# Kernel optimization log

Measured on AMD Instinct MI355X. Metric: run time of the kernel, lower is better.

The kernel has to match this reference:

```python
import jax, jax.numpy as jnp
import numpy as np

DEPTH, DIM, DH, QH, KH = 8, 512, 64, 16, 8
B, T, S = 2, 16, 257
NUM_SPECIAL, TBE, CLAMP = 1, 4, 50.0
DI = int(DIM * 4 * 2 / 3)  # 1365
EPS = 1.1920929e-07  # torch.finfo(float32).eps used by torch RMSNorm


def _rms(x, w):
    return x * jax.lax.rsqrt(jnp.mean(jnp.square(x), -1, keepdims=True) + EPS) * w


def _l2norm(x):
    return x / jnp.maximum(jnp.linalg.norm(x, axis=-1, keepdims=True), 1e-12)


def _rotary(n):
    inv = 1.0 / (10000.0 ** (jnp.arange(0, DH, 2, dtype=jnp.float32) / DH))
    f = jnp.arange(n, dtype=jnp.float32)[:, None] * inv[None, :]
    return jnp.concatenate([f, f], -1)  # [n, DH]


def _apply_rot(rot, x):
    x1, x2 = jnp.split(x, 2, -1)
    half = jnp.concatenate([-x2, x1], -1)
    return x * jnp.cos(rot) + half * jnp.sin(rot)


def _attend(q, k, v, mask=None, causal=False):
    # q: [b, QH, n, d]; k, v: [b, KH, n, d]; GQA with groups = QH//KH
    b, hq, n, d = q.shape
    h = k.shape[1]
    g = hq // h
    qg = q.reshape(b, h, g, n, d)
    sim = jnp.einsum('bhgid,bhjd->bhgij', qg, k) * (d ** -0.5)
    sim = jnp.tanh(sim / CLAMP) * CLAMP  # softclamp
    neg = -jnp.finfo(sim.dtype).max
    if mask is not None:
        sim = jnp.where(mask, sim, neg)
    if causal:
        j = sim.shape[-1]
        cm = jnp.triu(jnp.ones((n, j), bool), j - n + 1)
        sim = jnp.where(cm, neg, sim)
    attn = jax.nn.softmax(sim, axis=-1)
    out = jnp.einsum('bhgij,bhjd->bhgid', attn, v)
    return out.reshape(b, hq, n, d)


def _attn_block(x, nw, wq, wk, wv, qg, kg, wo, rot, mask, causal):
    bn, n, _ = x.shape
    h = _rms(x, nw)
    q = (h @ wq).reshape(bn, n, QH, DH).transpose(0, 2, 1, 3)
    k = (h @ wk).reshape(bn, n, KH, DH).transpose(0, 2, 1, 3)
    v = (h @ wv).reshape(bn, n, KH, DH).transpose(0, 2, 1, 3)
    sc = DH ** 0.5
    q = _l2norm(q) * ((qg + 1.0) * sc)[:, None, :]
    k = _l2norm(k) * ((kg + 1.0) * sc)[:, None, :]
    if rot is not None:
        q = _apply_rot(rot, q)
        k = _apply_rot(rot, k)
    o = _attend(q, k, v, mask=mask, causal=causal)
    o = o.transpose(0, 2, 1, 3).reshape(bn, n, QH * DH)
    return o @ wo


def _ff(x, nw, win, bin_, wout, bout):
    h = _rms(x, nw)
    a, g = jnp.split(h @ win + bin_, 2, -1)
    return (a * jax.nn.gelu(g, approximate=False)) @ wout + bout


def setup_inputs() -> dict:
    key = jax.random.key(0)
    ks = jax.random.split(key, 8)
    s = 0.02
    return {
        'tokens': jax.random.normal(ks[0], (B, T, S, DIM), jnp.float32),
        'attn_norm_w': jnp.ones((DEPTH, DIM), jnp.float32),
        'Wq': jax.random.normal(ks[1], (DEPTH, DIM, QH * DH), jnp.float32) * s,
        'Wk': jax.random.normal(ks[2], (DEPTH, DIM, KH * DH), jnp.float32) * s,
        'Wv': jax.random.normal(ks[3], (DEPTH, DIM, KH * DH), jnp.float32) * s,
        'q_gamma': jnp.zeros((DEPTH, QH, DH), jnp.float32),
        'k_gamma': jnp.zeros((DEPTH, KH, DH), jnp.float32),
        'Wo': jax.random.normal(ks[4], (DEPTH, QH * DH, DIM), jnp.float32) * s,
        'ff_norm_w': jnp.ones((DEPTH, DIM), jnp.float32),
        'W_in': jax.random.normal(ks[5], (DEPTH, DIM, 2 * DI), jnp.float32) * s,
        'b_in': jnp.zeros((DEPTH, 2 * DI), jnp.float32),
        'W_out': jax.random.normal(ks[6], (DEPTH, DI, DIM), jnp.float32) * s,
        'b_out': jnp.zeros((DEPTH, DIM), jnp.float32),
        'final_w': jnp.ones((DIM,), jnp.float32),
    }


def reference(tokens, attn_norm_w, Wq, Wk, Wv, q_gamma, k_gamma, Wo,
              ff_norm_w, W_in, b_in, W_out, b_out, final_w):
    x = tokens  # [B, T, S, D]
    # spatial special-token mask: normal tokens cannot attend to special (rightmost) tokens
    idx = jnp.arange(S)
    is_sp = idx >= (S - NUM_SPECIAL)
    sp_mask = ~((~is_sp[:, None]) & is_sp[None, :])  # [S, S]
    sp_mask = sp_mask[None, None, None]  # broadcast over (b, h, g)
    rot = _rotary(T)
    for l in range(DEPTH):
        is_time = (l + 1) % TBE == 0
        if is_time:
            y = x.transpose(0, 2, 1, 3).reshape(B * S, T, DIM)
            o = _attn_block(y, attn_norm_w[l], Wq[l], Wk[l], Wv[l], q_gamma[l],
                            k_gamma[l], Wo[l], rot=rot, mask=None, causal=True)
            x = x + o.reshape(B, S, T, DIM).transpose(0, 2, 1, 3)
        else:
            y = x.reshape(B * T, S, DIM)
            o = _attn_block(y, attn_norm_w[l], Wq[l], Wk[l], Wv[l], q_gamma[l],
                            k_gamma[l], Wo[l], rot=None, mask=sp_mask, causal=False)
            x = x + o.reshape(B, T, S, DIM)
        x = x + _ff(x, ff_norm_w[l], W_in[l], b_in[l], W_out[l], b_out[l])
    return _rms(x, final_w)
```

## Files before the change

kernel.cpp:

```cpp
#include <hip/hip_runtime.h>
#include <hip/hip_bf16.h>
#include <math.h>

typedef __attribute__((ext_vector_type(8))) short short8;
typedef __attribute__((ext_vector_type(4))) float f32x4;
typedef __hip_bfloat16 bf16;

#define BB 2
#define TT 16
#define SSQ 257
#define DIMD 512
#define NROWS 8224
#define DII 1365
#define DI2 2730
#define FNPAD 2816
#define GLULD 1408
#define SKP 288
#define EPSR 1.1920929e-07f

__device__ __forceinline__ void async16(const void* g, const void* l) {
    __builtin_amdgcn_global_load_lds(
        (const __attribute__((address_space(1))) void*)g,
        (__attribute__((address_space(3))) void*)l, 16, 0, 0);
}

__device__ __forceinline__ short f2bfs(float x) {
    bf16 h = __float2bfloat16(x);
    return *reinterpret_cast<short*>(&h);
}

__device__ __forceinline__ float glu_fast(float a, float g) {
    float x = g * 0.70710678118654752f;
    float ax = fabsf(x);
    float t = __builtin_amdgcn_rcpf(__builtin_fmaf(0.3275911f, ax, 1.f));
    float p = t * (0.254829592f + t * (-0.284496736f + t * (1.421413741f
              + t * (-1.453152027f + t * 1.061405429f))));
    float erfv = 1.f - p * __expf(-ax * ax);
    erfv = (x < 0.f) ? -erfv : erfv;
    return a * 0.5f * g * (1.f + erfv);
}

__global__ void wtrans_layer(const float* __restrict__ wq, const float* __restrict__ wk,
                             const float* __restrict__ wv, const float* __restrict__ wo,
                             const float* __restrict__ win, const float* __restrict__ wout,
                             bf16* __restrict__ dqkv, bf16* __restrict__ dwo,
                             bf16* __restrict__ dwin, bf16* __restrict__ dwout) {
    __shared__ float tile[32][33];
    int bid = blockIdx.x;
    const float* src; bf16* dst; int K, M, Kpad, interleave = 0, local;
    if (bid < 512)       { src = wq;   dst = dqkv;            K = 512;  M = 1024; Kpad = 512;  local = bid; }
    else if (bid < 768)  { src = wk;   dst = dqkv + 1024*512; K = 512;  M = 512;  Kpad = 512;  local = bid - 512; }
    else if (bid < 1024) { src = wv;   dst = dqkv + 1536*512; K = 512;  M = 512;  Kpad = 512;  local = bid - 768; }
    else if (bid < 1536) { src = wo;   dst = dwo;             K = 1024; M = 512;  Kpad = 1024; local = bid - 1024; }
    else if (bid < 2944) { src = win;  dst = dwin;            K = 512;  M = 2730; Kpad = 512;  local = bid - 1536; interleave = 1; }
    else                 { src = wout; dst = dwout;           K = 1365; M = 512;  Kpad = 1408; local = bid - 2944; }
    int tilesx = Kpad >> 5;
    int k0 = (local % tilesx) * 32, m0 = (local / tilesx) * 32;
    int tx = threadIdx.x & 31, ty = threadIdx.x >> 5;
    #pragma unroll
    for (int i = 0; i < 4; ++i) {
        int k = k0 + ty + 8 * i, m = m0 + tx;
        tile[ty + 8 * i][tx] = (k < K && m < M) ? src[(size_t)k * M + m] : 0.f;
    }
    __syncthreads();
    #pragma unroll
    for (int i = 0; i < 4; ++i) {
        int n = m0 + ty + 8 * i, k = k0 + tx;
        int nd = n;
        if (interleave) {
            if (n < DII)        nd = ((n >> 4) << 5) + (n & 15);
            else if (n < DI2) { int m = n - DII; nd = ((m >> 4) << 5) + 16 + (m & 15); }
            else              { int q = n - DI2; int j = DII + (q >> 1);
                                nd = ((j >> 4) << 5) + ((q & 1) << 4) + (j & 15); }
        }
        dst[(size_t)nd * Kpad + k] = __float2bfloat16(tile[tx][ty + 8 * i]);
    }
}

template<int BF16OUT>
__global__ __launch_bounds__(256)
void rms_kernel(const float* __restrict__ x, const float* __restrict__ w,
                void* __restrict__ out, int perm) {
    int wave = threadIdx.x >> 6, lane = threadIdx.x & 63;
    int r = blockIdx.x * 4 + wave;
    int src = r;
    if (perm) {
        int t = r & 15; int rs = r >> 4; int s = rs % SSQ; int b = rs / SSQ;
        src = (b * TT + t) * SSQ + s;
    }
    const float4* xr = (const float4*)(x + (size_t)src * DIMD) + lane * 2;
    float4 a = xr[0], c = xr[1];
    float ss = a.x*a.x + a.y*a.y + a.z*a.z + a.w*a.w
             + c.x*c.x + c.y*c.y + c.z*c.z + c.w*c.w;
    ss += __shfl_xor(ss, 1);  ss += __shfl_xor(ss, 2);  ss += __shfl_xor(ss, 4);
    ss += __shfl_xor(ss, 8);  ss += __shfl_xor(ss, 16); ss += __shfl_xor(ss, 32);
    float sc = rsqrtf(ss * (1.f / DIMD) + EPSR);
    const float4* wr = (const float4*)w + lane * 2;
    float4 wa = wr[0], wb = wr[1];
    if (BF16OUT) {
        short8 v;
        v[0] = f2bfs(a.x * sc * wa.x); v[1] = f2bfs(a.y * sc * wa.y);
        v[2] = f2bfs(a.z * sc * wa.z); v[3] = f2bfs(a.w * sc * wa.w);
        v[4] = f2bfs(c.x * sc * wb.x); v[5] = f2bfs(c.y * sc * wb.y);
        v[6] = f2bfs(c.z * sc * wb.z); v[7] = f2bfs(c.w * sc * wb.w);
        *(short8*)((bf16*)out + (size_t)r * DIMD + lane * 8) = v;
    } else {
        float4* o = (float4*)((float*)out + (size_t)r * DIMD) + lane * 2;
        float4 o0 = {a.x * sc * wa.x, a.y * sc * wa.y, a.z * sc * wa.z, a.w * sc * wa.w};
        float4 o1 = {c.x * sc * wb.x, c.y * sc * wb.y, c.z * sc * wb.z, c.w * sc * wb.w};
        o[0] = o0; o[1] = o1;
    }
}

template<int EPI>
__global__ __launch_bounds__(512, 1)
void mfma_gemm_panel(const bf16* __restrict__ A, int lda,
                     const bf16* __restrict__ Bt, int ldb,
                     const float* __restrict__ bias,
                     void* __restrict__ C, int ldc,
                     int nrow, int mchunk,
                     const float* __restrict__ qg, const float* __restrict__ kg,
                     int rotary) {
    __shared__ __align__(16) short lds_b[128 * 512];
    int gx = gridDim.x;
    int nwg = gx * gridDim.y;
    int lin = blockIdx.y * gx + blockIdx.x;
    int q8 = nwg >> 3, r8 = nwg & 7;
    int xcd = lin & 7, idx = lin >> 3;
    int wsw = (xcd < r8 ? xcd * (q8 + 1) : r8 * (q8 + 1) + (xcd - r8) * q8) + idx;
    int bx = wsw % gx, by = wsw / gx;
    int n0 = bx * 128, m0 = by * mchunk;

    int tid = threadIdx.x;
    int wave = tid >> 6, lane = tid & 63;
    int quad = lane >> 4, l16 = lane & 15;

    const short* Bp = (const short*)Bt;
    #pragma unroll
    for (int j = 0; j < 16; ++j) {
        int gi = tid + 512 * j;
        int n = gi & 127, c = gi >> 7;
        async16(Bp + (size_t)(n0 + n) * ldb + c * 8, &lds_b[gi * 8]);
    }
    const short* Ap = (const short*)A;

    float gl[2][4];
    float c0r[4], s0r[4], c1r[4], s1r[4];
    bool isqk = false;
    float ba[4], bg[4];
    if constexpr (EPI == 1) {
        int headb = n0 >> 6;
        isqk = headb < 24;
        if (isqk) {
            #pragma unroll
            for (int hh = 0; hh < 2; ++hh) {
                int head = headb + hh;
                const float* g = head < 16 ? qg + head * 64 : kg + (head - 16) * 64;
                gl[hh][0] = (g[l16] + 1.f) * 8.f;
                gl[hh][1] = (g[16 + l16] + 1.f) * 8.f;
                gl[hh][2] = (g[32 + l16] + 1.f) * 8.f;
                gl[hh][3] = (g[48 + l16] + 1.f) * 8.f;
            }
        }
        if (rotary) {
            float inv0 = __expf(-(float)l16 * 0.28782313662425572f);
            float inv1 = __expf(-(float)(l16 + 16) * 0.28782313662425572f);
            #pragma unroll
            for (int e = 0; e < 4; ++e) {
                float t = (float)(quad * 4 + e);
                c0r[e] = __cosf(t * inv0); s0r[e] = __sinf(t * inv0);
                c1r[e] = __cosf(t * inv1); s1r[e] = __sinf(t * inv1);
            }
        }
    } else {
        int jb = n0 >> 1;
        #pragma unroll
        for (int t = 0; t < 4; ++t) {
            int j = jb + t * 16 + l16;
            ba[t] = (j < DII) ? bias[j] : 0.f;
            bg[t] = (j < DII) ? bias[DII + j] : 0.f;
        }
    }
    __syncthreads();

    int base_b = (quad * 128 + l16) * 16;
    int nfrag = mchunk >> 4;
    for (int f = wave; f < nfrag; f += 8) {
        int mrow = m0 + f * 16 + l16;
        if (mrow >= nrow) mrow = nrow - 1;
        const short* ap = Ap + (size_t)mrow * lda + quad * 8;
        f32x4 acc[8];
        #pragma unroll
        for (int nj = 0; nj < 8; ++nj) acc[nj] = {0.f, 0.f, 0.f, 0.f};
        short8 a = *(const short8*)ap;
        short8 anext = a;
        #pragma unroll
        for (int kt = 0; kt < 16; ++kt) {
            if (kt < 15) anext = *(const short8*)(ap + (kt + 1) * 32);
            const char* vb = (const char*)lds_b + base_b + kt * 8192;
            __builtin_amdgcn_s_setprio(1);
            #pragma unroll
            for (int nj = 0; nj < 8; ++nj) {
                short8 b = *(const short8*)(vb + nj * 256);
                acc[nj] = __builtin_amdgcn_mfma_f32_16x16x32_bf16(a, b, acc[nj], 0, 0, 0);
            }
            __builtin_amdgcn_s_setprio(0);
            a = anext;
        }
        if constexpr (EPI == 1) {
            #pragma unroll
            for (int hh = 0; hh < 2; ++hh) {
                #pragma unroll
                for (int e = 0; e < 4; ++e) {
                    int row = m0 + f * 16 + quad * 4 + e;
                    float v0 = acc[hh * 4 + 0][e], v1 = acc[hh * 4 + 1][e];
                    float v2 = acc[hh * 4 + 2][e], v3 = acc[hh * 4 + 3][e];
                    if (isqk) {
                        float ss = v0 * v0 + v1 * v1 + v2 * v2 + v3 * v3;
                        ss += __shfl_xor(ss, 1); ss += __shfl_xor(ss, 2);
                        ss += __shfl_xor(ss, 4); ss += __shfl_xor(ss, 8);
                        float invn = 1.f / fmaxf(sqrtf(ss), 1e-12f);
                        v0 *= invn * gl[hh][0]; v1 *= invn * gl[hh][1];
                        v2 *= invn * gl[hh][2]; v3 *= invn * gl[hh][3];
                        if (rotary) {
                            float n0v = v0 * c0r[e] - v2 * s0r[e];
                            float n1v = v1 * c1r[e] - v3 * s1r[e];
                            float n2v = v2 * c0r[e] + v0 * s0r[e];
                            float n3v = v3 * c1r[e] + v1 * s1r[e];
                            v0 = n0v; v1 = n1v; v2 = n2v; v3 = n3v;
                        }
                    }
                    if (row < nrow) {
                        bf16* p = (bf16*)C + (size_t)row * ldc + n0 + hh * 64 + l16;
                        p[0]  = __float2bfloat16(v0);
                        p[16] = __float2bfloat16(v1);
                        p[32] = __float2bfloat16(v2);
                        p[48] = __float2bfloat16(v3);
                    }
                }
            }
        } else {
            int jb = n0 >> 1;
            #pragma unroll
            for (int e = 0; e < 4; ++e) {
                int row = m0 + f * 16 + quad * 4 + e;
                if (row < nrow) {
                    bf16* cr = (bf16*)C + (size_t)row * ldc;
                    #pragma unroll
                    for (int t = 0; t < 4; ++t)
                        cr[jb + t * 16 + l16] = __float2bfloat16(
                            glu_fast(acc[2 * t][e] + ba[t], acc[2 * t + 1][e] + bg[t]));
                }
            }
        }
    }
}

template<int EPI, int PERM, int TM>
__global__ __launch_bounds__(256)
void mfma_gemm(const bf16* __restrict__ A, int lda,
               const bf16* __restrict__ Bt, int ldb,
               const float* __restrict__ bias,
               void* __restrict__ C, int ldc, int Mstore,
               int nrow, int K) {
    constexpr int MI = TM / 32;
    constexpr int ALW = TM / 64;
    __shared__ __align__(16) short lds_a[2][TM * 32];
    __shared__ __align__(16) short lds_b[2][128 * 32];
    int tid = threadIdx.x;
    int wave = tid >> 6, lane = tid & 63;
    int quad = lane >> 4, l16 = lane & 15;
    int m0 = blockIdx.y * TM, n0 = blockIdx.x * 128;
    int wm = (wave & 1) * (TM / 2), wn = (wave >> 1) * 64;
    f32x4 zero4 = {0.f, 0.f, 0.f, 0.f};
    f32x4 acc[MI][4];
    #pragma unroll
    for (int i = 0; i < MI; ++i)
        #pragma unroll
        for (int j = 0; j < 4; ++j) acc[i][j] = zero4;

    const short* Ap = (const short*)A;
    const short* Bp = (const short*)Bt;
    auto aptr = [&](int g) {
        int m = g >> 2, kc = (g & 3) ^ ((g >> 3) & 3);
        int r = m0 + m; if (r >= nrow) r = nrow - 1;
        return Ap + (size_t)r * lda + kc * 8;
    };
    auto bptr = [&](int g) {
        int m = g >> 2, kc = (g & 3) ^ ((g >> 3) & 3);
        return Bp + (size_t)(n0 + m) * ldb + kc * 8;
    };
    const short* gA[ALW]; int aoff[ALW];
    #pragma unroll
    for (int j = 0; j < ALW; ++j) {
        gA[j] = aptr(wave * TM + j * 64 + lane);
        aoff[j] = (wave * TM + j * 64) * 8;
    }
    const short* gB0 = bptr(wave * 128 + lane);
    const short* gB1 = bptr(wave * 128 + 64 + lane);
    int boff0 = (wave * 128) * 8, boff1 = (wave * 128 + 64) * 8;

    auto stage = [&](int buf, int kt) {
        int ko = kt * 32;
        #pragma unroll
        for (int j = 0; j < ALW; ++j)
            async16(gA[j] + ko, &lds_a[buf][aoff[j]]);
        async16(gB0 + ko, &lds_b[buf][boff0]);
        async16(gB1 + ko, &lds_b[buf][boff1]);
    };

    int nk = K >> 5;
    stage(0, 0);
    for (int kt = 0; kt < nk; ++kt) {
        int buf = kt & 1;
        __syncthreads();
        if (kt + 1 < nk) stage(buf ^ 1, kt + 1);
        short8 af[MI], bfr[4];
        #pragma unroll
        for (int mi = 0; mi < MI; ++mi) {
            int m = wm + mi * 16 + l16;
            af[mi] = *(const short8*)&lds_a[buf][(m * 4 + (quad ^ ((m >> 1) & 3))) * 8];
        }
        #pragma unroll
        for (int nj = 0; nj < 4; ++nj) {
            int n = wn + nj * 16 + l16;
            bfr[nj] = *(const short8*)&lds_b[buf][(n * 4 + (quad ^ ((n >> 1) & 3))) * 8];
        }
        #pragma unroll
        for (int mi = 0; mi < MI; ++mi)
            #pragma unroll
            for (int nj = 0; nj < 4; ++nj)
                acc[mi][nj] = __builtin_amdgcn_mfma_f32_16x16x32_bf16(
                    af[mi], bfr[nj], acc[mi][nj], 0, 0, 0);
    }

    #pragma unroll
    for (int mi = 0; mi < MI; ++mi) {
        #pragma unroll
        for (int e = 0; e < 4; ++e) {
            int row = m0 + wm + mi * 16 + quad * 4 + e;
            if (row >= nrow) continue;
            int orow = row;
            if (PERM) {
                int t = row & 15; int rs = row >> 4; int s = rs % SSQ; int b = rs / SSQ;
                orow = (b * TT + t) * SSQ + s;
            }
            #pragma unroll
            for (int nj = 0; nj < 4; ++nj) {
                int col = n0 + wn + nj * 16 + l16;
                if (col >= Mstore) continue;
                float v = acc[mi][nj][e];
                if (bias) v += bias[col];
                ((float*)C)[(size_t)orow * ldc + col] += v;
            }
        }
    }
}

__global__ void vtrans_kernel(const bf16* __restrict__ qkv, bf16* __restrict__ vt) {
    int bkh = blockIdx.x;
    int kc = blockIdx.y;
    int bt = bkh >> 3, kh = bkh & 7;
    int tid = threadIdx.x;
    #pragma unroll
    for (int i = 0; i < 8; ++i) {
        int idx = tid + 256 * i;
        int kl = idx >> 6;
        int d = idx & 63;
        int key = kc * 32 + kl;
        float v = 0.f;
        if (key < SSQ)
            v = __bfloat162float(qkv[((size_t)(bt * SSQ + key)) * 2048 + 1536 + kh * 64 + d]);
        vt[((size_t)bkh * 64 + d) * SKP + key] = __float2bfloat16(v);
    }
}

__global__ __launch_bounds__(256)
void space_attn_kernel(const bf16* __restrict__ qkv, const bf16* __restrict__ vt,
                       bf16* __restrict__ ob) {
    __shared__ __align__(16) short kls[272 * 8 * 8];
    int qt = blockIdx.x, qh = blockIdx.y, bt = blockIdx.z;
    int kh = qh >> 1;
    int tid = threadIdx.x, wave = tid >> 6, lane = tid & 63;
    int quad = lane >> 4, l16 = lane & 15;
    int q0w = qt * 64 + wave * 16;
    int q = q0w + l16;
    int qc = q > 256 ? 256 : q;
    const short* qbase = (const short*)qkv + (size_t)bt * SSQ * 2048;

    const short* kgbase = qbase + 1024 + kh * 64;
    #pragma unroll
    for (int it = 0; it < 9; ++it) {
        int u = it * 4 + wave;
        if (u < 34) {
            int g = u * 64 + lane;
            int key = g >> 3, ch = g & 7;
            int srck = key < SSQ ? key : 256;
            async16(kgbase + (size_t)srck * 2048 + (ch ^ (key & 7)) * 8,
                    &kls[u * 512]);
        }
    }

    const short* qp = qbase + (size_t)qc * 2048 + qh * 64;
    short8 bq0 = *(const short8*)(qp + quad * 8);
    short8 bq1 = *(const short8*)(qp + 32 + quad * 8);
    __syncthreads();

    f32x4 zero4 = {0.f, 0.f, 0.f, 0.f};
    f32x4 sc[18];
    float sum = 0.f;
    int c0 = quad ^ (l16 & 7);
    #pragma unroll
    for (int kt = 0; kt < 17; ++kt) {
        int key = kt * 16 + l16;
        short8 ak0 = *(const short8*)&kls[(key * 8 + c0) * 8];
        short8 ak1 = *(const short8*)&kls[(key * 8 + (c0 ^ 4)) * 8];
        f32x4 cc = zero4;
        cc = __builtin_amdgcn_mfma_f32_16x16x32_bf16(ak0, bq0, cc, 0, 0, 0);
        cc = __builtin_amdgcn_mfma_f32_16x16x32_bf16(ak1, bq1, cc, 0, 0, 0);
        #pragma unroll
        for (int e = 0; e < 4; ++e) {
            float x = cc[e] * 0.0025f;
            float x2 = x * x;
            float v = cc[e] * 0.125f * (1.f + x2 * (-0.3333333333f + x2 * 0.1333333333f));
            float p = __expf(v);
            if (kt == 16) {
                bool valid = (e == 0) && (quad == 0) && (q == 256);
                p = valid ? p : 0.f;
            }
            cc[e] = p;
            sum += p;
        }
        sc[kt] = cc;
    }
    #pragma unroll
    for (int e = 0; e < 4; ++e) sc[17][e] = 0.f;
    sum += __shfl_xor(sum, 16);
    sum += __shfl_xor(sum, 32);
    float inv = __builtin_amdgcn_rcpf(sum);
    f32x4 inv4;
    #pragma unroll
    for (int e = 0; e < 4; ++e) inv4[e] = __shfl(inv, quad * 4 + e);

    f32x4 oacc[4];
    #pragma unroll
    for (int nt = 0; nt < 4; ++nt) oacc[nt] = zero4;
    const short* vbp = (const short*)vt + ((size_t)(bt * 8 + kh) * 64 + l16) * SKP;
    #pragma unroll
    for (int c8 = 0; c8 < 9; ++c8) {
        short8 pb;
        #pragma unroll
        for (int j = 0; j < 8; ++j) {
            int src_lane = ((quad & 1) * 2 + (j >> 2)) * 16 + l16;
            float v0 = __shfl(sc[2 * c8][j & 3], src_lane);
            float v1 = __shfl(sc[2 * c8 + 1][j & 3], src_lane);
            pb[j] = f2bfs(quad < 2 ? v0 : v1);
        }
        #pragma unroll
        for (int nt = 0; nt < 4; ++nt) {
            short8 av = *(const short8*)(vbp + (size_t)(nt * 16) * SKP + c8 * 32 + quad * 8);
            oacc[nt] = __builtin_amdgcn_mfma_f32_16x16x32_bf16(pb, av, oacc[nt], 0, 0, 0);
        }
    }

    #pragma unroll
    for (int e = 0; e < 4; ++e) {
        int qq = q0w + quad * 4 + e;
        if (qq <= 256) {
            bf16* op = ob + ((size_t)(bt * SSQ + qq)) * 1024 + qh * 64 + l16;
            float s = inv4[e];
            op[0]  = __float2bfloat16(oacc[0][e] * s);
            op[16] = __float2bfloat16(oacc[1][e] * s);
            op[32] = __float2bfloat16(oacc[2][e] * s);
            op[48] = __float2bfloat16(oacc[3][e] * s);
        }
    }
}

__global__ void time_attn_kernel(const bf16* __restrict__ qkv, bf16* __restrict__ ob) {
    __shared__ float qs[16][65], ks[16][65], ps[16][17];
    int bs = blockIdx.x, qh = blockIdx.y, kh = qh >> 1;
    int tid = threadIdx.x;
    size_t rowbase = (size_t)bs * 16;
    #pragma unroll
    for (int i = 0; i < 4; ++i) {
        int idx = tid + 256 * i;
        int r = idx >> 6, d = idx & 63;
        qs[r][d] = __bfloat162float(qkv[(rowbase + r) * 2048 + qh * 64 + d]);
        ks[r][d] = __bfloat162float(qkv[(rowbase + r) * 2048 + 1024 + kh * 64 + d]);
    }
    __syncthreads();
    int i = tid >> 4, j = tid & 15;
    float dot = 0.f;
    #pragma unroll 16
    for (int d = 0; d < 64; ++d) dot += qs[i][d] * ks[j][d];
    float s = dot * 0.125f;
    float x = s * 0.02f;
    float x2 = x * x;
    float v = s * (1.f + x2 * (-0.3333333333f + x2 * 0.1333333333f));
    float p = (j > i) ? 0.f : __expf(v);
    float sum = p;
    sum += __shfl_xor(sum, 1);
    sum += __shfl_xor(sum, 2);
    sum += __shfl_xor(sum, 4);
    sum += __shfl_xor(sum, 8);
    ps[i][j] = p * __builtin_amdgcn_rcpf(sum);
    __syncthreads();
    #pragma unroll
    for (int ii = 0; ii < 4; ++ii) {
        int idx = tid + 256 * ii;
        int r = idx >> 6, d = idx & 63;
        float acc = 0.f;
        #pragma unroll
        for (int jj = 0; jj < 16; ++jj)
            acc += ps[r][jj] * __bfloat162float(qkv[(rowbase + jj) * 2048 + 1536 + kh * 64 + d]);
        ob[(rowbase + r) * 1024 + qh * 64 + d] = __float2bfloat16(acc);
    }
}

extern "C" void kernel_launch(void* const* d_in, const int* in_sizes, int n_in,
                              void* d_out, int out_size, void* d_ws, size_t ws_size,
                              hipStream_t stream) {
    const float* tokens      = (const float*)d_in[0];
    const float* attn_norm_w = (const float*)d_in[1];
    const float* Wq          = (const float*)d_in[2];
    const float* Wk          = (const float*)d_in[3];
    const float* Wv          = (const float*)d_in[4];
    const float* q_gamma     = (const float*)d_in[5];
    const float* k_gamma     = (const float*)d_in[6];
    const float* Wo          = (const float*)d_in[7];
    const float* ff_norm_w   = (const float*)d_in[8];
    const float* W_in        = (const float*)d_in[9];
    const float* b_in        = (const float*)d_in[10];
    const float* W_out       = (const float*)d_in[11];
    const float* b_out       = (const float*)d_in[12];
    const float* final_w     = (const float*)d_in[13];

    float* x = (float*)d_out;
    char* ws = (char*)d_ws;

    bf16* wtqkv = (bf16*)ws;
    bf16* wto   = wtqkv + 2048 * 512;
    bf16* wtin  = wto   + 512 * 1024;
    bf16* wtout = wtin  + 2816 * 512;
    size_t off = (size_t)(2048*512 + 512*1024 + 2816*512 + 512*1408) * 2;
    bf16* h = (bf16*)(ws + off);
    off += (size_t)NROWS * 512 * 2;
    char* region = ws + off;
    bf16* qkv = (bf16*)region;
    bf16* glu = (bf16*)region;
    bf16* vt  = (bf16*)(region + (size_t)NROWS * 2048 * 2);
    bf16* ob  = (bf16*)(region + (size_t)NROWS * 2048 * 2 + (size_t)256*64*SKP*2);

    hipMemcpyAsync(x, tokens, (size_t)NROWS * 512 * 4, hipMemcpyDeviceToDevice, stream);

    for (int l = 0; l < 8; ++l) {
        int is_time = ((l + 1) % 4 == 0) ? 1 : 0;
        wtrans_layer<<<3648, 256, 0, stream>>>(
            Wq + (size_t)l * 512 * 1024, Wk + (size_t)l * 512 * 512,
            Wv + (size_t)l * 512 * 512, Wo + (size_t)l * 1024 * 512,
            W_in + (size_t)l * 512 * DI2, W_out + (size_t)l * DII * 512,
            wtqkv, wto, wtin, wtout);

        rms_kernel<1><<<2056, 256, 0, stream>>>(x, attn_norm_w + (size_t)l * 512, h, is_time);
        mfma_gemm_panel<1><<<dim3(16, 16), 512, 0, stream>>>(
            h, 512, wtqkv, 512, nullptr, qkv, 2048, NROWS, 528,
            q_gamma + (size_t)l * 1024, k_gamma + (size_t)l * 512, is_time);
        if (is_time) {
            time_attn_kernel<<<dim3(514, 16), 256, 0, stream>>>(qkv, ob);
            mfma_gemm<3, 1, 64><<<dim3(4, 129), 256, 0, stream>>>(
                ob, 1024, wto, 1024, nullptr, x, 512, 512, NROWS, 1024);
        } else {
            vtrans_kernel<<<dim3(256, 9), 256, 0, stream>>>(qkv, vt);
            space_attn_kernel<<<dim3(5, 16, 32), 256, 0, stream>>>(qkv, vt, ob);
            mfma_gemm<3, 0, 64><<<dim3(4, 129), 256, 0, stream>>>(
                ob, 1024, wto, 1024, nullptr, x, 512, 512, NROWS, 1024);
        }

        rms_kernel<1><<<2056, 256, 0, stream>>>(x, ff_norm_w + (size_t)l * 512, h, 0);
        mfma_gemm_panel<2><<<dim3(22, 11), 512, 0, stream>>>(
            h, 512, wtin, 512, b_in + (size_t)l * DI2, glu, GLULD, NROWS, 768,
            nullptr, nullptr, 0);
        mfma_gemm<3, 0, 64><<<dim3(4, 129), 256, 0, stream>>>(
            glu, GLULD, wtout, GLULD, b_out + (size_t)l * 512, x, 512, 512, NROWS, GLULD);
    }

    rms_kernel<0><<<2056, 256, 0, stream>>>(x, final_w, x, 0);
}
```

Before: 2.057 ms.

## Replace accumulate GEMMs with LDS-resident B panel kernel and MFMA time attention

The output-projection and FF-down GEMMs now use a new kernel that loads a 64-column slice of the transposed weight fully into LDS (up to 128KB). Each wave then streams A rows directly from global memory with register prefetch, and workgroups are swizzled across XCDs. The FF-down GEMM is split into two K-chunk launches (1024 + 384) because of the LDS size limit, and both accumulate into x in fp32. The time attention kernel is rewritten to use MFMA for QK^T and PV, with four heads per block and K/V staged in LDS. This replaces the scalar LDS dot products. The trade-off is single-block occupancy per CU, and the split launches add an extra read-modify-write of x.

```diff
diff --git a/kernel.cpp b/kernel.cpp
--- a/kernel.cpp
+++ b/kernel.cpp
@@ -256,103 +256,76 @@
     }
 }
 
-template<int EPI, int PERM, int TM>
-__global__ __launch_bounds__(256)
-void mfma_gemm(const bf16* __restrict__ A, int lda,
-               const bf16* __restrict__ Bt, int ldb,
-               const float* __restrict__ bias,
-               void* __restrict__ C, int ldc, int Mstore,
-               int nrow, int K) {
-    constexpr int MI = TM / 32;
-    constexpr int ALW = TM / 64;
-    __shared__ __align__(16) short lds_a[2][TM * 32];
-    __shared__ __align__(16) short lds_b[2][128 * 32];
+__global__ __launch_bounds__(512, 1)
+void mfma_panel_acc(const bf16* __restrict__ A, int lda, int koff, int K,
+                    const bf16* __restrict__ Bt, int ldb,
+                    const float* __restrict__ bias,
+                    float* __restrict__ C, int ldc,
+                    int nrow, int mchunk, int perm) {
+    __shared__ __align__(16) short lds_b[64 * 1024];
+    int gx = gridDim.x;
+    int nwg = gx * gridDim.y;
+    int lin = blockIdx.y * gx + blockIdx.x;
+    int q8 = nwg >> 3, r8 = nwg & 7;
+    int xcd = lin & 7, idx = lin >> 3;
+    int wsw = (xcd < r8 ? xcd * (q8 + 1) : r8 * (q8 + 1) + (xcd - r8) * q8) + idx;
+    int bx = wsw % gx, by = wsw / gx;
+    int n0 = bx * 64, m0 = by * mchunk;
+
     int tid = threadIdx.x;
     int wave = tid >> 6, lane = tid & 63;
     int quad = lane >> 4, l16 = lane & 15;
-    int m0 = blockIdx.y * TM, n0 = blockIdx.x * 128;
-    int wm = (wave & 1) * (TM / 2), wn = (wave >> 1) * 64;
-    f32x4 zero4 = {0.f, 0.f, 0.f, 0.f};
-    f32x4 acc[MI][4];
-    #pragma unroll
-    for (int i = 0; i < MI; ++i)
-        #pragma unroll
-        for (int j = 0; j < 4; ++j) acc[i][j] = zero4;
+
+    const short* Bp = (const short*)Bt;
+    int ng = (K >> 3) * 64;
+    for (int gi = tid; gi < ng; gi += 512) {
+        int n = gi & 63, c = gi >> 6;
+        async16(Bp + (size_t)(n0 + n) * ldb + koff + c * 8, &lds_b[gi * 8]);
+    }
+    float bs4[4];
+    #pragma unroll
+    for (int t = 0; t < 4; ++t)
+        bs4[t] = bias ? bias[n0 + t * 16 + l16] : 0.f;
+    __syncthreads();
 
     const short* Ap = (const short*)A;
-    const short* Bp = (const short*)Bt;
-    auto aptr = [&](int g) {
-        int m = g >> 2, kc = (g & 3) ^ ((g >> 3) & 3);
-        int r = m0 + m; if (r >= nrow) r = nrow - 1;
-        return Ap + (size_t)r * lda + kc * 8;
-    };
-    auto bptr = [&](int g) {
-        int m = g >> 2, kc = (g & 3) ^ ((g >> 3) & 3);
-        return Bp + (size_t)(n0 + m) * ldb + kc * 8;
-    };
-    const short* gA[ALW]; int aoff[ALW];
-    #pragma unroll
-    for (int j = 0; j < ALW; ++j) {
-        gA[j] = aptr(wave * TM + j * 64 + lane);
-        aoff[j] = (wave * TM + j * 64) * 8;
-    }
-    const short* gB0 = bptr(wave * 128 + lane);
-    const short* gB1 = bptr(wave * 128 + 64 + lane);
-    int boff0 = (wave * 128) * 8, boff1 = (wave * 128 + 64) * 8;
-
-    auto stage = [&](int buf, int kt) {
-        int ko = kt * 32;
-        #pragma unroll
-        for (int j = 0; j < ALW; ++j)
-            async16(gA[j] + ko, &lds_a[buf][aoff[j]]);
-        async16(gB0 + ko, &lds_b[buf][boff0]);
-        async16(gB1 + ko, &lds_b[buf][boff1]);
-    };
-
     int nk = K >> 5;
-    stage(0, 0);
-    for (int kt = 0; kt < nk; ++kt) {
-        int buf = kt & 1;
-        __syncthreads();
-        if (kt + 1 < nk) stage(buf ^ 1, kt + 1);
-        short8 af[MI], bfr[4];
-        #pragma unroll
-        for (int mi = 0; mi < MI; ++mi) {
-            int m = wm + mi * 16 + l16;
-            af[mi] = *(const short8*)&lds_a[buf][(m * 4 + (quad ^ ((m >> 1) & 3))) * 8];
-        }
-        #pragma unroll
-        for (int nj = 0; nj < 4; ++nj) {
-            int n = wn + nj * 16 + l16;
-            bfr[nj] = *(const short8*)&lds_b[buf][(n * 4 + (quad ^ ((n >> 1) & 3))) * 8];
-        }
-        #pragma unroll
-        for (int mi = 0; mi < MI; ++mi)
+    int nfrag = mchunk >> 4;
+    for (int f = wave; f < nfrag; f += 8) {
+        int mrow = m0 + f * 16 + l16;
+        if (mrow >= nrow) mrow = nrow - 1;
+        const short* ap = Ap + (size_t)mrow * lda + koff + quad * 8;
+        f32x4 acc[4];
+        #pragma unroll
+        for (int nj = 0; nj < 4; ++nj) acc[nj] = {0.f, 0.f, 0.f, 0.f};
+        short8 a = *(const short8*)ap;
+        #pragma unroll 4
+        for (int kt = 0; kt < nk; ++kt) {
+            short8 anext = a;
+            if (kt + 1 < nk) anext = *(const short8*)(ap + (kt + 1) * 32);
+            const char* vb = (const char*)lds_b + ((kt * 4 + quad) * 64 + l16) * 16;
+            __builtin_amdgcn_s_setprio(1);
+            #pragma unroll
+            for (int nj = 0; nj < 4; ++nj) {
+                short8 b = *(const short8*)(vb + nj * 256);
+                acc[nj] = __builtin_amdgcn_mfma_f32_16x16x32_bf16(a, b, acc[nj], 0, 0, 0);
+            }
+            __builtin_amdgcn_s_setprio(0);
+            a = anext;
+        }
+        #pragma unroll
+        for (int e = 0; e < 4; ++e) {
+            int row = m0 + f * 16 + quad * 4 + e;
+            if (row >= nrow) continue;
+            int orow = row;
+            if (perm) {
+                int t = row & 15; int rs = row >> 4; int s = rs % SSQ; int b = rs / SSQ;
+                orow = (b * TT + t) * SSQ + s;
+            }
+            float* cr = C + (size_t)orow * ldc + n0;
             #pragma unroll
             for (int nj = 0; nj < 4; ++nj)
-                acc[mi][nj] = __builtin_amdgcn_mfma_f32_16x16x32_bf16(
-                    af[mi], bfr[nj], acc[mi][nj], 0, 0, 0);
-    }
-
-    #pragma unroll
-    for (int mi = 0; mi < MI; ++mi) {
-        #pragma unroll
-        for (int e = 0; e < 4; ++e) {
-            int row = m0 + wm + mi * 16 + quad * 4 + e;
-            if (row >= nrow) continue;
-            int orow = row;
-            if (PERM) {
-                int t = row & 15; int rs = row >> 4; int s = rs % SSQ; int b = rs / SSQ;
-                orow = (b * TT + t) * SSQ + s;
-            }
-            #pragma unroll
-            for (int nj = 0; nj < 4; ++nj) {
-                int col = n0 + wn + nj * 16 + l16;
-                if (col >= Mstore) continue;
-                float v = acc[mi][nj][e];
-                if (bias) v += bias[col];
-                ((float*)C)[(size_t)orow * ldc + col] += v;
-            }
+                cr[nj * 16 + l16] += acc[nj][e] + bs4[nj];
         }
     }
 }
@@ -477,44 +450,86 @@
     }
 }
 
-__global__ void time_attn_kernel(const bf16* __restrict__ qkv, bf16* __restrict__ ob) {
-    __shared__ float qs[16][65], ks[16][65], ps[16][17];
-    int bs = blockIdx.x, qh = blockIdx.y, kh = qh >> 1;
-    int tid = threadIdx.x;
+__global__ __launch_bounds__(256)
+void time_attn_kernel(const bf16* __restrict__ qkv, bf16* __restrict__ ob) {
+    __shared__ __align__(16) short kls[2 * 16 * 64];
+    __shared__ __align__(16) short vls[2 * 64 * 24];
+    int bs = blockIdx.x, qg = blockIdx.y;
+    int tid = threadIdx.x, wave = tid >> 6, lane = tid & 63;
+    int quad = lane >> 4, l16 = lane & 15;
+    int qh = qg * 4 + wave;
+    int khl_w = wave >> 1;
     size_t rowbase = (size_t)bs * 16;
-    #pragma unroll
-    for (int i = 0; i < 4; ++i) {
-        int idx = tid + 256 * i;
-        int r = idx >> 6, d = idx & 63;
-        qs[r][d] = __bfloat162float(qkv[(rowbase + r) * 2048 + qh * 64 + d]);
-        ks[r][d] = __bfloat162float(qkv[(rowbase + r) * 2048 + 1024 + kh * 64 + d]);
-    }
+    const short* qbase = (const short*)qkv;
+
+    {
+        int c = tid & 7, key = (tid >> 3) & 15, khl = tid >> 7;
+        const short* ksrc = qbase + (rowbase + key) * 2048 + 1024 + (qg * 2 + khl) * 64
+                            + (c ^ (key & 7)) * 8;
+        async16(ksrc, &kls[((khl * 16 + key) * 8 + c) * 8]);
+        short8 vv = *(const short8*)(qbase + (rowbase + key) * 2048 + 1536
+                                     + (qg * 2 + khl) * 64 + c * 8);
+        #pragma unroll
+        for (int dd = 0; dd < 8; ++dd)
+            vls[(khl * 64 + c * 8 + dd) * 24 + key] = vv[dd];
+    }
+    const short* qp = qbase + (rowbase + l16) * 2048 + qh * 64;
+    short8 bq0 = *(const short8*)(qp + quad * 8);
+    short8 bq1 = *(const short8*)(qp + 32 + quad * 8);
     __syncthreads();
-    int i = tid >> 4, j = tid & 15;
-    float dot = 0.f;
-    #pragma unroll 16
-    for (int d = 0; d < 64; ++d) dot += qs[i][d] * ks[j][d];
-    float s = dot * 0.125f;
-    float x = s * 0.02f;
-    float x2 = x * x;
-    float v = s * (1.f + x2 * (-0.3333333333f + x2 * 0.1333333333f));
-    float p = (j > i) ? 0.f : __expf(v);
-    float sum = p;
-    sum += __shfl_xor(sum, 1);
-    sum += __shfl_xor(sum, 2);
-    sum += __shfl_xor(sum, 4);
-    sum += __shfl_xor(sum, 8);
-    ps[i][j] = p * __builtin_amdgcn_rcpf(sum);
-    __syncthreads();
-    #pragma unroll
-    for (int ii = 0; ii < 4; ++ii) {
-        int idx = tid + 256 * ii;
-        int r = idx >> 6, d = idx & 63;
-        float acc = 0.f;
-        #pragma unroll
-        for (int jj = 0; jj < 16; ++jj)
-            acc += ps[r][jj] * __bfloat162float(qkv[(rowbase + jj) * 2048 + 1536 + kh * 64 + d]);
-        ob[(rowbase + r) * 1024 + qh * 64 + d] = __float2bfloat16(acc);
+
+    int c0 = quad ^ (l16 & 7);
+    const short* kw = &kls[(khl_w * 16 + l16) * 64];
+    short8 ak0 = *(const short8*)(kw + c0 * 8);
+    short8 ak1 = *(const short8*)(kw + (c0 ^ 4) * 8);
+    f32x4 cc = {0.f, 0.f, 0.f, 0.f};
+    cc = __builtin_amdgcn_mfma_f32_16x16x32_bf16(ak0, bq0, cc, 0, 0, 0);
+    cc = __builtin_amdgcn_mfma_f32_16x16x32_bf16(ak1, bq1, cc, 0, 0, 0);
+    float sum = 0.f;
+    #pragma unroll
+    for (int e = 0; e < 4; ++e) {
+        float s = cc[e] * 0.125f;
+        float x = s * 0.02f, x2 = x * x;
+        float v = s * (1.f + x2 * (-0.3333333333f + x2 * 0.1333333333f));
+        float p = ((quad * 4 + e) > l16) ? 0.f : __expf(v);
+        cc[e] = p;
+        sum += p;
+    }
+    sum += __shfl_xor(sum, 16);
+    sum += __shfl_xor(sum, 32);
+    float inv = __builtin_amdgcn_rcpf(sum);
+    f32x4 inv4;
+    #pragma unroll
+    for (int e = 0; e < 4; ++e) inv4[e] = __shfl(inv, quad * 4 + e);
+
+    short8 pa;
+    #pragma unroll
+    for (int jj = 0; jj < 8; ++jj) {
+        int key = quad * 8 + jj;
+        int src = ((key >> 2) & 3) * 16 + l16;
+        float v = __shfl(cc[jj & 3], src);
+        pa[jj] = f2bfs(quad < 2 ? v : 0.f);
+    }
+    const short* vw = &vls[khl_w * 64 * 24];
+    short8 zero8 = {0, 0, 0, 0, 0, 0, 0, 0};
+    f32x4 oacc[4];
+    #pragma unroll
+    for (int nt = 0; nt < 4; ++nt) {
+        short8 av = zero8;
+        if (quad < 2)
+            av = *(const short8*)(vw + (nt * 16 + l16) * 24 + quad * 8);
+        f32x4 z = {0.f, 0.f, 0.f, 0.f};
+        oacc[nt] = __builtin_amdgcn_mfma_f32_16x16x32_bf16(pa, av, z, 0, 0, 0);
+    }
+    #pragma unroll
+    for (int e = 0; e < 4; ++e) {
+        int q = quad * 4 + e;
+        bf16* op = ob + (rowbase + q) * 1024 + qh * 64 + l16;
+        float s = inv4[e];
+        op[0]  = __float2bfloat16(oacc[0][e] * s);
+        op[16] = __float2bfloat16(oacc[1][e] * s);
+        op[32] = __float2bfloat16(oacc[2][e] * s);
+        op[48] = __float2bfloat16(oacc[3][e] * s);
     }
 }
 
@@ -567,22 +582,24 @@
             h, 512, wtqkv, 512, nullptr, qkv, 2048, NROWS, 528,
             q_gamma + (size_t)l * 1024, k_gamma + (size_t)l * 512, is_time);
         if (is_time) {
-            time_attn_kernel<<<dim3(514, 16), 256, 0, stream>>>(qkv, ob);
-            mfma_gemm<3, 1, 64><<<dim3(4, 129), 256, 0, stream>>>(
-                ob, 1024, wto, 1024, nullptr, x, 512, 512, NROWS, 1024);
+            time_attn_kernel<<<dim3(514, 4), 256, 0, stream>>>(qkv, ob);
         } else {
             vtrans_kernel<<<dim3(256, 9), 256, 0, stream>>>(qkv, vt);
             space_attn_kernel<<<dim3(5, 16, 32), 256, 0, stream>>>(qkv, vt, ob);
-            mfma_gemm<3, 0, 64><<<dim3(4, 129), 256, 0, stream>>>(
-                ob, 1024, wto, 1024, nullptr, x, 512, 512, NROWS, 1024);
-        }
+        }
+        mfma_panel_acc<<<dim3(8, 31), 512, 0, stream>>>(
+            ob, 1024, 0, 1024, wto, 1024, nullptr, x, 512, NROWS, 272, is_time);
 
         rms_kernel<1><<<2056, 256, 0, stream>>>(x, ff_norm_w + (size_t)l * 512, h, 0);
         mfma_gemm_panel<2><<<dim3(22, 11), 512, 0, stream>>>(
             h, 512, wtin, 512, b_in + (size_t)l * DI2, glu, GLULD, NROWS, 768,
             nullptr, nullptr, 0);
-        mfma_gemm<3, 0, 64><<<dim3(4, 129), 256, 0, stream>>>(
-            glu, GLULD, wtout, GLULD, b_out + (size_t)l * 512, x, 512, 512, NROWS, GLULD);
+        mfma_panel_acc<<<dim3(8, 31), 512, 0, stream>>>(
+            glu, GLULD, 0, 1024, wtout, GLULD, b_out + (size_t)l * 512, x, 512,
+            NROWS, 272, 0);
+        mfma_panel_acc<<<dim3(8, 31), 512, 0, stream>>>(
+            glu, GLULD, 1024, 384, wtout, GLULD, nullptr, x, 512,
+            NROWS, 272, 0);
     }
 
     rms_kernel<0><<<2056, 256, 0, stream>>>(x, final_w, x, 0);
```

Measured after the change: 2.142 ms. 4.1% more time.

## Fuse V transpose into space attention and rewrite time attention with MFMA

Applied to the files above, without the earlier changes.

The space attention kernel now loads K and transposes V into LDS itself, which removes the separate vtrans kernel and its global round trip. Each block covers one (bt, kh) pair and loops over both query heads of the GQA group, so K/V are staged once per group instead of once per query tile and head. The time attention kernel is rewritten to use bf16 MFMA for QK^T and PV, with one block serving four query heads, in place of the scalar fp32 LDS loops. The costs are fewer blocks for the space kernel (256), larger LDS per block, and a scalar scatter when transposing V.

```diff
diff --git a/kernel.cpp b/kernel.cpp
--- a/kernel.cpp
+++ b/kernel.cpp
@@ -16,6 +16,7 @@
 #define FNPAD 2816
 #define GLULD 1408
 #define SKP 288
+#define SKP2 320
 #define EPSR 1.1920929e-07f
 
 __device__ __forceinline__ void async16(const void* g, const void* l) {
@@ -357,84 +358,177 @@
     }
 }
 
-__global__ void vtrans_kernel(const bf16* __restrict__ qkv, bf16* __restrict__ vt) {
-    int bkh = blockIdx.x;
-    int kc = blockIdx.y;
-    int bt = bkh >> 3, kh = bkh & 7;
-    int tid = threadIdx.x;
-    #pragma unroll
-    for (int i = 0; i < 8; ++i) {
-        int idx = tid + 256 * i;
-        int kl = idx >> 6;
-        int d = idx & 63;
-        int key = kc * 32 + kl;
-        float v = 0.f;
-        if (key < SSQ)
-            v = __bfloat162float(qkv[((size_t)(bt * SSQ + key)) * 2048 + 1536 + kh * 64 + d]);
-        vt[((size_t)bkh * 64 + d) * SKP + key] = __float2bfloat16(v);
-    }
-}
-
-__global__ __launch_bounds__(256)
-void space_attn_kernel(const bf16* __restrict__ qkv, const bf16* __restrict__ vt,
-                       bf16* __restrict__ ob) {
+__global__ __launch_bounds__(512)
+void space_attn_kernel(const bf16* __restrict__ qkv, bf16* __restrict__ ob) {
     __shared__ __align__(16) short kls[272 * 8 * 8];
-    int qt = blockIdx.x, qh = blockIdx.y, bt = blockIdx.z;
-    int kh = qh >> 1;
+    __shared__ __align__(16) short vls[64 * SKP2];
+    int bt = blockIdx.x, kh = blockIdx.y;
     int tid = threadIdx.x, wave = tid >> 6, lane = tid & 63;
     int quad = lane >> 4, l16 = lane & 15;
-    int q0w = qt * 64 + wave * 16;
-    int q = q0w + l16;
-    int qc = q > 256 ? 256 : q;
     const short* qbase = (const short*)qkv + (size_t)bt * SSQ * 2048;
-
     const short* kgbase = qbase + 1024 + kh * 64;
-    #pragma unroll
-    for (int it = 0; it < 9; ++it) {
-        int u = it * 4 + wave;
-        if (u < 34) {
-            int g = u * 64 + lane;
+    const short* vgbase = qbase + 1536 + kh * 64;
+
+    #pragma unroll
+    for (int u = 0; u < 5; ++u) {
+        int g = u * 512 + tid;
+        if (g < 2176) {
             int key = g >> 3, ch = g & 7;
             int srck = key < SSQ ? key : 256;
-            async16(kgbase + (size_t)srck * 2048 + (ch ^ (key & 7)) * 8,
-                    &kls[u * 512]);
-        }
-    }
-
-    const short* qp = qbase + (size_t)qc * 2048 + qh * 64;
+            async16(kgbase + (size_t)srck * 2048 + (ch ^ (key & 7)) * 8, &kls[g * 8]);
+        }
+    }
+    #pragma unroll
+    for (int u = 0; u < 5; ++u) {
+        int g = u * 512 + tid;
+        if (g < 2176) {
+            int key = g >> 3, c = g & 7;
+            int srck = key < SSQ ? key : 256;
+            short8 vv = *(const short8*)(vgbase + (size_t)srck * 2048 + c * 8);
+            int kc = key >> 3, kl = key & 7;
+            #pragma unroll
+            for (int dd = 0; dd < 8; ++dd) {
+                int d = c * 8 + dd;
+                vls[(d * 40 + (kc ^ (d & 7))) * 8 + kl] = vv[dd];
+            }
+        }
+    }
+    if (tid < 128) {
+        int d = tid >> 1, kc = 34 + (tid & 1);
+        short8 z8 = {0, 0, 0, 0, 0, 0, 0, 0};
+        *(short8*)&vls[(d * 40 + (kc ^ (d & 7))) * 8] = z8;
+    }
+    __syncthreads();
+
+    f32x4 zero4 = {0.f, 0.f, 0.f, 0.f};
+    int c0 = quad ^ (l16 & 7);
+    int d7 = l16 & 7;
+    for (int f = wave; f < 34; f += 8) {
+        int qh_l = (f >= 17) ? 1 : 0;
+        int qt = f - qh_l * 17;
+        int qh = kh * 2 + qh_l;
+        int q = qt * 16 + l16;
+        int qc = q > 256 ? 256 : q;
+        const short* qp = qbase + (size_t)qc * 2048 + qh * 64;
+        short8 bq0 = *(const short8*)(qp + quad * 8);
+        short8 bq1 = *(const short8*)(qp + 32 + quad * 8);
+
+        f32x4 sc[18];
+        float sum = 0.f;
+        #pragma unroll
+        for (int kt = 0; kt < 17; ++kt) {
+            int key = kt * 16 + l16;
+            short8 ak0 = *(const short8*)&kls[(key * 8 + c0) * 8];
+            short8 ak1 = *(const short8*)&kls[(key * 8 + (c0 ^ 4)) * 8];
+            f32x4 cc = zero4;
+            cc = __builtin_amdgcn_mfma_f32_16x16x32_bf16(ak0, bq0, cc, 0, 0, 0);
+            cc = __builtin_amdgcn_mfma_f32_16x16x32_bf16(ak1, bq1, cc, 0, 0, 0);
+            #pragma unroll
+            for (int e = 0; e < 4; ++e) {
+                float x = cc[e] * 0.0025f;
+                float x2 = x * x;
+                float v = cc[e] * 0.125f * (1.f + x2 * (-0.3333333333f + x2 * 0.1333333333f));
+                float p = __expf(v);
+                if (kt == 16) {
+                    bool valid = (e == 0) && (quad == 0) && (q == 256);
+                    p = valid ? p : 0.f;
+                }
+                cc[e] = p;
+                sum += p;
+            }
+            sc[kt] = cc;
+        }
+        #pragma unroll
+        for (int e = 0; e < 4; ++e) sc[17][e] = 0.f;
+        sum += __shfl_xor(sum, 16);
+        sum += __shfl_xor(sum, 32);
+        float inv = __builtin_amdgcn_rcpf(sum);
+        f32x4 inv4;
+        #pragma unroll
+        for (int e = 0; e < 4; ++e) inv4[e] = __shfl(inv, quad * 4 + e);
+
+        f32x4 oacc[4];
+        #pragma unroll
+        for (int nt = 0; nt < 4; ++nt) oacc[nt] = zero4;
+        #pragma unroll
+        for (int c8 = 0; c8 < 9; ++c8) {
+            short8 pb;
+            #pragma unroll
+            for (int j = 0; j < 8; ++j) {
+                int src_lane = ((quad & 1) * 2 + (j >> 2)) * 16 + l16;
+                float v0 = __shfl(sc[2 * c8][j & 3], src_lane);
+                float v1 = __shfl(sc[2 * c8 + 1][j & 3], src_lane);
+                pb[j] = f2bfs(quad < 2 ? v0 : v1);
+            }
+            #pragma unroll
+            for (int nt = 0; nt < 4; ++nt) {
+                int d = nt * 16 + l16;
+                int kc = (c8 * 4 + quad) ^ d7;
+                short8 av = *(const short8*)&vls[(d * 40 + kc) * 8];
+                oacc[nt] = __builtin_amdgcn_mfma_f32_16x16x32_bf16(pb, av, oacc[nt], 0, 0, 0);
+            }
+        }
+
+        #pragma unroll
+        for (int e = 0; e < 4; ++e) {
+            int qq = qt * 16 + quad * 4 + e;
+            if (qq <= 256) {
+                bf16* op = ob + ((size_t)(bt * SSQ + qq)) * 1024 + qh * 64 + l16;
+                float s = inv4[e];
+                op[0]  = __float2bfloat16(oacc[0][e] * s);
+                op[16] = __float2bfloat16(oacc[1][e] * s);
+                op[32] = __float2bfloat16(oacc[2][e] * s);
+                op[48] = __float2bfloat16(oacc[3][e] * s);
+            }
+        }
+    }
+}
+
+__global__ __launch_bounds__(256)
+void time_attn_kernel(const bf16* __restrict__ qkv, bf16* __restrict__ ob) {
+    __shared__ __align__(16) short kls[2 * 16 * 64];
+    __shared__ __align__(16) short vls[2 * 64 * 24];
+    int bs = blockIdx.x, qg = blockIdx.y;
+    int tid = threadIdx.x, wave = tid >> 6, lane = tid & 63;
+    int quad = lane >> 4, l16 = lane & 15;
+    int qh = qg * 4 + wave;
+    int khl_w = wave >> 1;
+    size_t rowbase = (size_t)bs * 16;
+    const short* qbase = (const short*)qkv;
+
+    {
+        int c = tid & 7, key = (tid >> 3) & 15, khl = tid >> 7;
+        const short* ksrc = qbase + (rowbase + key) * 2048 + 1024 + (qg * 2 + khl) * 64
+                            + (c ^ (key & 7)) * 8;
+        async16(ksrc, &kls[((khl * 16 + key) * 8 + c) * 8]);
+        short8 vv = *(const short8*)(qbase + (rowbase + key) * 2048 + 1536
+                                     + (qg * 2 + khl) * 64 + c * 8);
+        #pragma unroll
+        for (int dd = 0; dd < 8; ++dd)
+            vls[(khl * 64 + c * 8 + dd) * 24 + key] = vv[dd];
+    }
+    const short* qp = qbase + (rowbase + l16) * 2048 + qh * 64;
     short8 bq0 = *(const short8*)(qp + quad * 8);
     short8 bq1 = *(const short8*)(qp + 32 + quad * 8);
     __syncthreads();
 
-    f32x4 zero4 = {0.f, 0.f, 0.f, 0.f};
-    f32x4 sc[18];
+    int c0 = quad ^ (l16 & 7);
+    const short* kw = &kls[(khl_w * 16 + l16) * 64];
+    short8 ak0 = *(const short8*)(kw + c0 * 8);
+    short8 ak1 = *(const short8*)(kw + (c0 ^ 4) * 8);
+    f32x4 cc = {0.f, 0.f, 0.f, 0.f};
+    cc = __builtin_amdgcn_mfma_f32_16x16x32_bf16(ak0, bq0, cc, 0, 0, 0);
+    cc = __builtin_amdgcn_mfma_f32_16x16x32_bf16(ak1, bq1, cc, 0, 0, 0);
     float sum = 0.f;
-    int c0 = quad ^ (l16 & 7);
-    #pragma unroll
-    for (int kt = 0; kt < 17; ++kt) {
-        int key = kt * 16 + l16;
-        short8 ak0 = *(const short8*)&kls[(key * 8 + c0) * 8];
-        short8 ak1 = *(const short8*)&kls[(key * 8 + (c0 ^ 4)) * 8];
-        f32x4 cc = zero4;
-        cc = __builtin_amdgcn_mfma_f32_16x16x32_bf16(ak0, bq0, cc, 0, 0, 0);
-        cc = __builtin_amdgcn_mfma_f32_16x16x32_bf16(ak1, bq1, cc, 0, 0, 0);
-        #pragma unroll
-        for (int e = 0; e < 4; ++e) {
-            float x = cc[e] * 0.0025f;
-            float x2 = x * x;
-            float v = cc[e] * 0.125f * (1.f + x2 * (-0.3333333333f + x2 * 0.1333333333f));
-            float p = __expf(v);
-            if (kt == 16) {
-                bool valid = (e == 0) && (quad == 0) && (q == 256);
-                p = valid ? p : 0.f;
-            }
-            cc[e] = p;
-            sum += p;
-        }
-        sc[kt] = cc;
-    }
-    #pragma unroll
-    for (int e = 0; e < 4; ++e) sc[17][e] = 0.f;
+    #pragma unroll
+    for (int e = 0; e < 4; ++e) {
+        float s = cc[e] * 0.125f;
+        float x = s * 0.02f, x2 = x * x;
+        float v = s * (1.f + x2 * (-0.3333333333f + x2 * 0.1333333333f));
+        float p = ((quad * 4 + e) > l16) ? 0.f : __expf(v);
+        cc[e] = p;
+        sum += p;
+    }
     sum += __shfl_xor(sum, 16);
     sum += __shfl_xor(sum, 32);
     float inv = __builtin_amdgcn_rcpf(sum);
@@ -442,79 +536,34 @@
     #pragma unroll
     for (int e = 0; e < 4; ++e) inv4[e] = __shfl(inv, quad * 4 + e);
 
+    short8 pa;
+    #pragma unroll
+    for (int jj = 0; jj < 8; ++jj) {
+        int key = quad * 8 + jj;
+        int src = ((key >> 2) & 3) * 16 + l16;
+        float v = __shfl(cc[jj & 3], src);
+        pa[jj] = f2bfs(quad < 2 ? v : 0.f);
+    }
+    const short* vw = &vls[khl_w * 64 * 24];
+    short8 zero8 = {0, 0, 0, 0, 0, 0, 0, 0};
     f32x4 oacc[4];
     #pragma unroll
-    for (int nt = 0; nt < 4; ++nt) oacc[nt] = zero4;
-    const short* vbp = (const short*)vt + ((size_t)(bt * 8 + kh) * 64 + l16) * SKP;
-    #pragma unroll
-    for (int c8 = 0; c8 < 9; ++c8) {
-        short8 pb;
-        #pragma unroll
-        for (int j = 0; j < 8; ++j) {
-            int src_lane = ((quad & 1) * 2 + (j >> 2)) * 16 + l16;
-            float v0 = __shfl(sc[2 * c8][j & 3], src_lane);
-            float v1 = __shfl(sc[2 * c8 + 1][j & 3], src_lane);
-            pb[j] = f2bfs(quad < 2 ? v0 : v1);
-        }
-        #pragma unroll
-        for (int nt = 0; nt < 4; ++nt) {
-            short8 av = *(const short8*)(vbp + (size_t)(nt * 16) * SKP + c8 * 32 + quad * 8);
-            oacc[nt] = __builtin_amdgcn_mfma_f32_16x16x32_bf16(pb, av, oacc[nt], 0, 0, 0);
-        }
-    }
-
+    for (int nt = 0; nt < 4; ++nt) {
+        short8 av = zero8;
+        if (quad < 2)
+            av = *(const short8*)(vw + (nt * 16 + l16) * 24 + quad * 8);
+        f32x4 z = {0.f, 0.f, 0.f, 0.f};
+        oacc[nt] = __builtin_amdgcn_mfma_f32_16x16x32_bf16(pa, av, z, 0, 0, 0);
+    }
     #pragma unroll
     for (int e = 0; e < 4; ++e) {
-        int qq = q0w + quad * 4 + e;
-        if (qq <= 256) {
-            bf16* op = ob + ((size_t)(bt * SSQ + qq)) * 1024 + qh * 64 + l16;
-            float s = inv4[e];
-            op[0]  = __float2bfloat16(oacc[0][e] * s);
-            op[16] = __float2bfloat16(oacc[1][e] * s);
-            op[32] = __float2bfloat16(oacc[2][e] * s);
-            op[48] = __float2bfloat16(oacc[3][e] * s);
-        }
-    }
-}
-
-__global__ void time_attn_kernel(const bf16* __restrict__ qkv, bf16* __restrict__ ob) {
-    __shared__ float qs[16][65], ks[16][65], ps[16][17];
-    int bs = blockIdx.x, qh = blockIdx.y, kh = qh >> 1;
-    int tid = threadIdx.x;
-    size_t rowbase = (size_t)bs * 16;
-    #pragma unroll
-    for (int i = 0; i < 4; ++i) {
-        int idx = tid + 256 * i;
-        int r = idx >> 6, d = idx & 63;
-        qs[r][d] = __bfloat162float(qkv[(rowbase + r) * 2048 + qh * 64 + d]);
-        ks[r][d] = __bfloat162float(qkv[(rowbase + r) * 2048 + 1024 + kh * 64 + d]);
-    }
-    __syncthreads();
-    int i = tid >> 4, j = tid & 15;
-    float dot = 0.f;
-    #pragma unroll 16
-    for (int d = 0; d < 64; ++d) dot += qs[i][d] * ks[j][d];
-    float s = dot * 0.125f;
-    float x = s * 0.02f;
-    float x2 = x * x;
-    float v = s * (1.f + x2 * (-0.3333333333f + x2 * 0.1333333333f));
-    float p = (j > i) ? 0.f : __expf(v);
-    float sum = p;
-    sum += __shfl_xor(sum, 1);
-    sum += __shfl_xor(sum, 2);
-    sum += __shfl_xor(sum, 4);
-    sum += __shfl_xor(sum, 8);
-    ps[i][j] = p * __builtin_amdgcn_rcpf(sum);
-    __syncthreads();
-    #pragma unroll
-    for (int ii = 0; ii < 4; ++ii) {
-        int idx = tid + 256 * ii;
-        int r = idx >> 6, d = idx & 63;
-        float acc = 0.f;
-        #pragma unroll
-        for (int jj = 0; jj < 16; ++jj)
-            acc += ps[r][jj] * __bfloat162float(qkv[(rowbase + jj) * 2048 + 1536 + kh * 64 + d]);
-        ob[(rowbase + r) * 1024 + qh * 64 + d] = __float2bfloat16(acc);
+        int q = quad * 4 + e;
+        bf16* op = ob + (rowbase + q) * 1024 + qh * 64 + l16;
+        float s = inv4[e];
+        op[0]  = __float2bfloat16(oacc[0][e] * s);
+        op[16] = __float2bfloat16(oacc[1][e] * s);
+        op[32] = __float2bfloat16(oacc[2][e] * s);
+        op[48] = __float2bfloat16(oacc[3][e] * s);
     }
 }
 
@@ -549,7 +598,6 @@
     char* region = ws + off;
     bf16* qkv = (bf16*)region;
     bf16* glu = (bf16*)region;
-    bf16* vt  = (bf16*)(region + (size_t)NROWS * 2048 * 2);
     bf16* ob  = (bf16*)(region + (size_t)NROWS * 2048 * 2 + (size_t)256*64*SKP*2);
 
     hipMemcpyAsync(x, tokens, (size_t)NROWS * 512 * 4, hipMemcpyDeviceToDevice, stream);
@@ -567,12 +615,11 @@
             h, 512, wtqkv, 512, nullptr, qkv, 2048, NROWS, 528,
             q_gamma + (size_t)l * 1024, k_gamma + (size_t)l * 512, is_time);
         if (is_time) {
-            time_attn_kernel<<<dim3(514, 16), 256, 0, stream>>>(qkv, ob);
+            time_attn_kernel<<<dim3(514, 4), 256, 0, stream>>>(qkv, ob);
             mfma_gemm<3, 1, 64><<<dim3(4, 129), 256, 0, stream>>>(
                 ob, 1024, wto, 1024, nullptr, x, 512, 512, NROWS, 1024);
         } else {
-            vtrans_kernel<<<dim3(256, 9), 256, 0, stream>>>(qkv, vt);
-            space_attn_kernel<<<dim3(5, 16, 32), 256, 0, stream>>>(qkv, vt, ob);
+            space_attn_kernel<<<dim3(32, 8), 512, 0, stream>>>(qkv, ob);
             mfma_gemm<3, 0, 64><<<dim3(4, 129), 256, 0, stream>>>(
                 ob, 1024, wto, 1024, nullptr, x, 512, 512, NROWS, 1024);
         }
```

Result: faster. 1.958 ms (-4.8%).
